# Performance work log

Measured on AMD Instinct MI355X. Metric: run time of the kernel, lower is better.

## Reference

```python
import jax, jax.numpy as jnp
import numpy as np

DIM = 1024
N_HEADS = 16
HEAD_DIM = DIM // N_HEADS
ROPE_BASE = 10000.0


def setup_inputs() -> dict:
    key = jax.random.key(0)
    ks = jax.random.split(key, 5)
    B, T = 4, 2048
    s_in = 1.0 / np.sqrt(DIM)
    x = jax.random.normal(ks[0], (B, T, DIM), dtype=jnp.float32)
    W_qkv = jax.random.uniform(ks[1], (DIM, 3 * DIM), jnp.float32, -s_in, s_in)
    b_qkv = jax.random.uniform(ks[2], (3 * DIM,), jnp.float32, -s_in, s_in)
    W_proj = jax.random.uniform(ks[3], (DIM, DIM), jnp.float32, -s_in, s_in)
    b_proj = jax.random.uniform(ks[4], (DIM,), jnp.float32, -s_in, s_in)
    return {"x": x, "W_qkv": W_qkv, "b_qkv": b_qkv, "W_proj": W_proj, "b_proj": b_proj}


def _rope_cos_sin(T, dtype):
    inv_freq = 1.0 / (ROPE_BASE ** (jnp.arange(0, HEAD_DIM, 2, dtype=jnp.float32) / HEAD_DIM))
    t = jnp.arange(T, dtype=jnp.float32)
    freqs = jnp.outer(t, inv_freq)            # (T, HEAD_DIM/2)
    emb = jnp.concatenate([freqs, freqs], -1)  # (T, HEAD_DIM)
    return jnp.cos(emb).astype(dtype), jnp.sin(emb).astype(dtype)


def _rotate_half(x):
    x1, x2 = jnp.split(x, 2, axis=-1)
    return jnp.concatenate([-x2, x1], axis=-1)


def reference(x, W_qkv, b_qkv, W_proj, b_proj):
    B, T, C = x.shape
    qkv = x @ W_qkv + b_qkv                              # (B, T, 3C)
    qkv = qkv.reshape(B, T, 3, N_HEADS, HEAD_DIM)
    qkv = jnp.transpose(qkv, (2, 0, 3, 1, 4))            # (3, B, H, T, d)
    q, k, v = qkv[0], qkv[1], qkv[2]
    cos, sin = _rope_cos_sin(T, x.dtype)
    cos = cos[None, None]                                # (1,1,T,d)
    sin = sin[None, None]
    q = q * cos + _rotate_half(q) * sin
    k = k * cos + _rotate_half(k) * sin
    scale = 1.0 / np.sqrt(HEAD_DIM)
    scores = jnp.einsum('bhqd,bhkd->bhqk', q, k) * scale  # (B,H,T,T)
    attn = jax.nn.softmax(scores, axis=-1)
    out = jnp.einsum('bhqk,bhkd->bhqd', attn, v)          # (B,H,T,d)
    out = jnp.transpose(out, (0, 2, 1, 3)).reshape(B, T, C)
    return out @ W_proj + b_proj
```

## Files before the change

### kernel.cpp

```cpp
#include <hip/hip_runtime.h>
#include <hip/hip_bf16.h>
#include <cstdint>
#include <cstddef>

typedef __bf16 bf16x8 __attribute__((ext_vector_type(8)));
typedef float f32x4 __attribute__((ext_vector_type(4)));
typedef float f32x16 __attribute__((ext_vector_type(16)));
typedef unsigned short ushort8 __attribute__((ext_vector_type(8)));

#define MFMA16(a, b, c) __builtin_amdgcn_mfma_f32_16x16x32_bf16(a, b, c, 0, 0, 0)
#define MFMA32(a, b, c) __builtin_amdgcn_mfma_f32_32x32x16_bf16(a, b, c, 0, 0, 0)

__device__ __forceinline__ void gll16(const void* g, void* l) {
  __builtin_amdgcn_global_load_lds((__attribute__((address_space(1))) unsigned int*)g,
                                   (__attribute__((address_space(3))) unsigned int*)l,
                                   16, 0, 0);
}

__device__ __forceinline__ float exp2_raw(float x) {
  return __builtin_amdgcn_exp2f(x);
}

__device__ __forceinline__ bf16x8 pack8(float a0, float a1, float a2, float a3,
                                        float a4, float a5, float a6, float a7) {
  unsigned w0, w1, w2, w3;
  asm("v_cvt_pk_bf16_f32 %0, %1, %2" : "=v"(w0) : "v"(a0), "v"(a1));
  asm("v_cvt_pk_bf16_f32 %0, %1, %2" : "=v"(w1) : "v"(a2), "v"(a3));
  asm("v_cvt_pk_bf16_f32 %0, %1, %2" : "=v"(w2) : "v"(a4), "v"(a5));
  asm("v_cvt_pk_bf16_f32 %0, %1, %2" : "=v"(w3) : "v"(a6), "v"(a7));
  asm("v_permlane32_swap_b32 %0, %1" : "+v"(w0), "+v"(w2));
  asm("v_permlane32_swap_b32 %0, %1" : "+v"(w1), "+v"(w3));
  union { unsigned u[4]; bf16x8 v; } r;
  r.u[0] = w0; r.u[1] = w1; r.u[2] = w2; r.u[3] = w3;
  return r.v;
}


__global__ void cvt_x(const float* __restrict__ in, __bf16* __restrict__ out) {
  int i = (blockIdx.x * 256 + threadIdx.x) * 8;
  float4 a = *(const float4*)(in + i);
  float4 c = *(const float4*)(in + i + 4);
  bf16x8 r;
  r[0] = (__bf16)a.x; r[1] = (__bf16)a.y; r[2] = (__bf16)a.z; r[3] = (__bf16)a.w;
  r[4] = (__bf16)c.x; r[5] = (__bf16)c.y; r[6] = (__bf16)c.z; r[7] = (__bf16)c.w;
  *(bf16x8*)(out + i) = r;
}

__global__ void rope_tab_k(float2* __restrict__ tab) {
  int i = blockIdx.x * 256 + threadIdx.x;
  int t = i >> 5, ii = i & 31;
  float invf = exp2f(-(float)ii * (13.287712379549449f / 32.0f));
  float a = (float)t * invf;
  tab[i] = make_float2(cosf(a), sinf(a));
}

__global__ void transp_bf16(const float* __restrict__ W, __bf16* __restrict__ Wt,
                            int K, int N) {
  __shared__ float tile[32][33];
  int n0 = blockIdx.x * 32, k0 = blockIdx.y * 32;
  int tx = threadIdx.x & 31, ty = threadIdx.x >> 5;
  #pragma unroll
  for (int r = ty; r < 32; r += 8)
    tile[r][tx] = W[(size_t)(k0 + r) * N + n0 + tx];
  __syncthreads();
  #pragma unroll
  for (int r = ty; r < 32; r += 8)
    Wt[(size_t)(n0 + r) * K + k0 + tx] = (__bf16)tile[tx][r];
}

__global__ void transp_v(const __bf16* __restrict__ in, __bf16* __restrict__ out) {
  __shared__ unsigned short tile[64][72];
  const int bh = blockIdx.y, t0 = blockIdx.x * 64;
  const int tid = threadIdx.x;
  const int r = tid >> 3, c = (tid & 7) * 8;
  const __bf16* src = in + ((size_t)bh * 2048 + t0) * 64;
  ushort8 a = *(const ushort8*)(src + (size_t)r * 64 + c);
  ushort8 b = *(const ushort8*)(src + (size_t)(r + 32) * 64 + c);
  #pragma unroll
  for (int e = 0; e < 8; ++e) { tile[c + e][r] = a[e]; tile[c + e][r + 32] = b[e]; }
  __syncthreads();
  const int d = tid >> 3, tc = tid & 7;
  __bf16* dst0 = out + ((size_t)bh * 64 + d) * 2048 + t0;
  *(ushort8*)(dst0 + tc * 8) = *(const ushort8*)&tile[d][tc * 8];
  __bf16* dst1 = out + ((size_t)bh * 64 + d + 32) * 2048 + t0;
  *(ushort8*)(dst1 + tc * 8) = *(const ushort8*)&tile[d + 32][tc * 8];
}

template <int EPI>
__global__ __launch_bounds__(256, 4) void gemm_bt(
    const __bf16* __restrict__ A, const __bf16* __restrict__ Bt,
    const float* __restrict__ bias, float* __restrict__ Cf,
    __bf16* __restrict__ qp, __bf16* __restrict__ kp, __bf16* __restrict__ vp,
    const float2* __restrict__ ctab, int M, int N, int K) {
  __shared__ __align__(16) char smem[32768];
  const int tid = threadIdx.x;
  const int w = tid >> 6, l = tid & 63, l15 = l & 15, g = l >> 4;
  const int wr = w >> 1, wc = w & 1;
  const int brow = blockIdx.y * 128, bcol = blockIdx.x * 128;

  f32x4 acc[4][4] = {};
  const int rsub = tid >> 3;
  const int sf   = (rsub & 7) ^ (((rsub >> 3) & 3) << 1);
  const int schunk = (((tid & 7) ^ sf) << 4);

  const int fr0 = (l15 & 7) ^ (((l15 >> 3) & 3) << 1);
  const int fr1 = (l15 & 7) ^ ((((l15 >> 3) + 2) & 3) << 1);

  for (int kt = 0; kt < K; kt += 64) {
    __syncthreads();
    #pragma unroll
    for (int i = 0; i < 4; ++i) {
      const char* ga = (const char*)(A + (size_t)(brow + i * 32 + rsub) * K + kt) + schunk;
      gll16(ga, smem + i * 4096 + tid * 16);
      const char* gb = (const char*)(Bt + (size_t)(bcol + i * 32 + rsub) * K + kt) + schunk;
      gll16(gb, smem + 16384 + i * 4096 + tid * 16);
    }
    __syncthreads();
    #pragma unroll
    for (int kk = 0; kk < 2; ++kk) {
      bf16x8 af[4], bfr[4];
      #pragma unroll
      for (int m = 0; m < 4; ++m) {
        int fx = (m & 1) ? fr1 : fr0;
        af[m] = *(const bf16x8*)(smem + (wr * 64 + m * 16 + l15) * 128 +
                                 (((kk * 4 + g) ^ fx) << 4));
      }
      #pragma unroll
      for (int n = 0; n < 4; ++n) {
        int fx = (n & 1) ? fr1 : fr0;
        bfr[n] = *(const bf16x8*)(smem + 16384 + (wc * 64 + n * 16 + l15) * 128 +
                                  (((kk * 4 + g) ^ fx) << 4));
      }
      __builtin_amdgcn_s_setprio(1);
      #pragma unroll
      for (int m = 0; m < 4; ++m)
        #pragma unroll
        for (int n = 0; n < 4; ++n)
          acc[m][n] = MFMA16(af[m], bfr[n], acc[m][n]);
      __builtin_amdgcn_s_setprio(0);
    }
  }

  const int colb = bcol + wc * 64;
  float bs[4];
  #pragma unroll
  for (int n = 0; n < 4; ++n) bs[n] = bias[colb + n * 16 + l15];

  if (EPI == 1) {
    #pragma unroll
    for (int m = 0; m < 4; ++m)
      #pragma unroll
      for (int j = 0; j < 4; ++j) {
        int row = brow + wr * 64 + m * 16 + g * 4 + j;
        float* crow = Cf + (size_t)row * N + colb;
        #pragma unroll
        for (int n = 0; n < 4; ++n)
          crow[n * 16 + l15] = acc[m][n][j] + bs[n];
      }
  } else {
    const int which = colb >> 10;
    const int h = (colb & 1023) >> 6;
    __bf16* dst = (which == 0) ? qp : (which == 1) ? kp : vp;
    const float SCLQ = 0.18033688011112042f;
    #pragma unroll
    for (int m = 0; m < 4; ++m)
      #pragma unroll
      for (int j = 0; j < 4; ++j) {
        int row = brow + wr * 64 + m * 16 + g * 4 + j;
        int bb = row >> 11, t = row & 2047;
        float v0 = acc[m][0][j] + bs[0];
        float v1 = acc[m][1][j] + bs[1];
        float v2 = acc[m][2][j] + bs[2];
        float v3 = acc[m][3][j] + bs[3];
        if (which < 2) {
          float2 cs0 = ctab[t * 32 + l15];
          float2 cs1 = ctab[t * 32 + 16 + l15];
          float r0 = v0 * cs0.x - v2 * cs0.y;
          float r2 = v2 * cs0.x + v0 * cs0.y;
          float r1 = v1 * cs1.x - v3 * cs1.y;
          float r3 = v3 * cs1.x + v1 * cs1.y;
          v0 = r0; v1 = r1; v2 = r2; v3 = r3;
        }
        if (which == 0) { v0 *= SCLQ; v1 *= SCLQ; v2 *= SCLQ; v3 *= SCLQ; }
        __bf16* orow = dst + ((size_t)(bb * 16 + h) * 2048 + t) * 64;
        orow[l15]      = (__bf16)v0;
        orow[16 + l15] = (__bf16)v1;
        orow[32 + l15] = (__bf16)v2;
        orow[48 + l15] = (__bf16)v3;
      }
  }
}

__global__ __launch_bounds__(256, 4) void flash_attn(
    const __bf16* __restrict__ q, const __bf16* __restrict__ k,
    const __bf16* __restrict__ vt, __bf16* __restrict__ o) {
  __shared__ __align__(16) char smem[32768];
  const int id = blockIdx.x;
  const int nid = (id & 7) * 128 + (id >> 3);
  const int bh = nid >> 4, qb = nid & 15;
  const int b = bh >> 4, h = bh & 15;
  const int tid = threadIdx.x, w = tid >> 6, l = tid & 63;
  const int l31 = l & 31, hi = l >> 5;

  const char* kbase  = (const char*)(k  + (size_t)bh * 2048 * 64);
  const char* vtbase = (const char*)(vt + (size_t)bh * 64 * 2048);

  bf16x8 qf[4];
  const int qrow0 = qb * 128 + w * 32;
  #pragma unroll
  for (int ks = 0; ks < 4; ++ks)
    qf[ks] = *(const bf16x8*)(q + (size_t)bh * 2048 * 64 +
                              (size_t)(qrow0 + l31) * 64 + ks * 16 + hi * 8);

  f32x16 accO[2] = {};
  float lr = 0.f;

  const int koff[2] = { 0, 16384 };
  const int voff[2] = { 8192, 24576 };

  const int srow = tid >> 3;
  const int ssw  = (((tid & 7) ^ ((tid >> 3) & 7) ^ (((tid >> 6) & 3) << 1)) << 4);
  const int swz  = (((l & 7) ^ (((l >> 3) & 3) << 1)) << 4);

  gll16(kbase + srow * 128 + ssw,                  smem + koff[0] + tid * 16);
  gll16(kbase + (srow + 32) * 128 + ssw,           smem + koff[0] + 4096 + tid * 16);
  gll16(vtbase + (size_t)srow * 4096 + ssw,        smem + voff[0] + tid * 16);
  gll16(vtbase + (size_t)(srow + 32) * 4096 + ssw, smem + voff[0] + 4096 + tid * 16);
  __syncthreads();

  for (int t = 0; t < 32; ++t) {
    const int cur = t & 1;
    char* Kc = smem + koff[cur];
    char* Vc = smem + voff[cur];
    if (t < 31) {
      char* Kn = smem + koff[cur ^ 1];
      char* Vn = smem + voff[cur ^ 1];
      const char* gk = kbase + (size_t)(t + 1) * 8192;
      gll16(gk + srow * 128 + ssw,        Kn + tid * 16);
      gll16(gk + (srow + 32) * 128 + ssw, Kn + 4096 + tid * 16);
      const char* gv = vtbase + (size_t)(t + 1) * 128;
      gll16(gv + (size_t)srow * 4096 + ssw,        Vn + tid * 16);
      gll16(gv + (size_t)(srow + 32) * 4096 + ssw, Vn + 4096 + tid * 16);
    }

    f32x16 st0 = {}, st1 = {};
    __builtin_amdgcn_s_setprio(1);
    #pragma unroll
    for (int ks = 0; ks < 4; ++ks) {
      bf16x8 kf0 = *(const bf16x8*)(Kc + (l31) * 128 + ((ks * 32 + hi * 16) ^ swz));
      bf16x8 kf1 = *(const bf16x8*)(Kc + (32 + l31) * 128 + ((ks * 32 + hi * 16) ^ swz));
      st0 = MFMA32(kf0, qf[ks], st0);
      st1 = MFMA32(kf1, qf[ks], st1);
    }
    __builtin_amdgcn_s_setprio(0);

    bf16x8 pa[4];
    {
      float p[16];
      #pragma unroll
      for (int r = 0; r < 16; ++r) p[r] = exp2_raw(st0[r]);
      lr += (((p[0] + p[1]) + (p[2] + p[3])) + ((p[4] + p[5]) + (p[6] + p[7]))) +
            (((p[8] + p[9]) + (p[10] + p[11])) + ((p[12] + p[13]) + (p[14] + p[15])));
      pa[0] = pack8(p[0], p[1], p[2], p[3], p[4], p[5], p[6], p[7]);
      pa[1] = pack8(p[8], p[9], p[10], p[11], p[12], p[13], p[14], p[15]);
    }
    {
      float p[16];
      #pragma unroll
      for (int r = 0; r < 16; ++r) p[r] = exp2_raw(st1[r]);
      lr += (((p[0] + p[1]) + (p[2] + p[3])) + ((p[4] + p[5]) + (p[6] + p[7]))) +
            (((p[8] + p[9]) + (p[10] + p[11])) + ((p[12] + p[13]) + (p[14] + p[15])));
      pa[2] = pack8(p[0], p[1], p[2], p[3], p[4], p[5], p[6], p[7]);
      pa[3] = pack8(p[8], p[9], p[10], p[11], p[12], p[13], p[14], p[15]);
    }

    __builtin_amdgcn_s_setprio(1);
    #pragma unroll
    for (int ks = 0; ks < 4; ++ks) {
      bf16x8 vf0 = *(const bf16x8*)(Vc + (l31) * 128 + ((ks * 32 + hi * 16) ^ swz));
      bf16x8 vf1 = *(const bf16x8*)(Vc + (32 + l31) * 128 + ((ks * 32 + hi * 16) ^ swz));
      accO[0] = MFMA32(pa[ks], vf0, accO[0]);
      accO[1] = MFMA32(pa[ks], vf1, accO[1]);
    }
    __builtin_amdgcn_s_setprio(0);
    __syncthreads();
  }

  float lrf = lr + __shfl_xor(lr, 32);
  __bf16* obase = o + (size_t)(b * 2048) * 1024 + h * 64;
  #pragma unroll
  for (int r = 0; r < 16; ++r) {
    int qloc = (r & 3) + 8 * (r >> 2) + 4 * hi;
    float inv = 1.0f / __shfl(lrf, qloc);
    __bf16* orow = obase + (size_t)(qrow0 + qloc) * 1024;
    orow[l31]      = (__bf16)(accO[0][r] * inv);
    orow[32 + l31] = (__bf16)(accO[1][r] * inv);
  }
}


extern "C" void kernel_launch(void* const* d_in, const int* in_sizes, int n_in,
                              void* d_out, int out_size, void* d_ws, size_t ws_size,
                              hipStream_t stream) {
  const float* x     = (const float*)d_in[0];
  const float* Wqkv  = (const float*)d_in[1];
  const float* bqkv  = (const float*)d_in[2];
  const float* Wproj = (const float*)d_in[3];
  const float* bproj = (const float*)d_in[4];
  float* out = (float*)d_out;

  char* ws = (char*)d_ws;
  __bf16* xb  = (__bf16*)(ws);
  __bf16* wtq = (__bf16*)(ws + 16777216);
  __bf16* wtp = (__bf16*)(ws + 23068672);
  __bf16* qp  = (__bf16*)(ws + 25165824);
  __bf16* kp  = (__bf16*)(ws + 41943040);
  __bf16* vp  = (__bf16*)(ws + 58720256);
  __bf16* ao  = (__bf16*)(ws + 75497472);
  float2* ct  = (float2*)(ws + 92274688);
  __bf16* vtp = xb;
  if (ws_size < 92798976) return;

  cvt_x<<<4096, 256, 0, stream>>>(x, xb);
  rope_tab_k<<<256, 256, 0, stream>>>(ct);
  transp_bf16<<<dim3(96, 32), 256, 0, stream>>>(Wqkv, wtq, 1024, 3072);
  transp_bf16<<<dim3(32, 32), 256, 0, stream>>>(Wproj, wtp, 1024, 1024);
  gemm_bt<0><<<dim3(24, 64), 256, 0, stream>>>(xb, wtq, bqkv, nullptr, qp, kp, vp, ct,
                                               8192, 3072, 1024);
  transp_v<<<dim3(32, 64), 256, 0, stream>>>(vp, vtp);
  flash_attn<<<1024, 256, 0, stream>>>(qp, kp, vtp, ao);
  gemm_bt<1><<<dim3(8, 64), 256, 0, stream>>>(ao, wtp, bproj, out, nullptr, nullptr,
                                              nullptr, nullptr, 8192, 1024, 1024);
}
```

Measured before the change: 196.0 us.

## Replace QKV GEMM with 256x256 8-wave ping-pong pipelined kernel

Adds a new QKV projection GEMM that uses 256x256 tiles, 512 threads and 128 KB of dynamic LDS split into two buffers. Each buffer holds 64-wide K tiles in quadrant halves, and loads for upcoming tiles are interleaved with MFMA compute on the current quadrants under explicit barriers and vmcnt waits. It also remaps workgroup IDs across 8 groups (XCD-aware) and raises MFMA priority. The goal is more data reuse per tile and hiding global-to-LDS latency. In exchange, occupancy drops to one block per CU and the grid shrinks to 384 blocks, which may cause tail or underfill effects on 256 CUs.

```diff
diff --git a/kernel.cpp b/kernel.cpp
--- a/kernel.cpp
+++ b/kernel.cpp
@@ -86,6 +86,184 @@
   *(ushort8*)(dst1 + tc * 8) = *(const ushort8*)&tile[d + 32][tc * 8];
 }
 
+
+template <int QM, int QN>
+__device__ __forceinline__ void compute_quad(
+    const char* buf, f32x4 (&acc)[2][2][2][4],
+    int wrp, int wcp, int l15, int g, int fr0, int fr1) {
+  const char* Ar = buf + QM * 16384;
+  const char* Br = buf + 32768 + QN * 16384;
+  bf16x8 af[2][2], bfr[4][2];
+  #pragma unroll
+  for (int m = 0; m < 2; ++m) {
+    int fx = (m & 1) ? fr1 : fr0;
+    #pragma unroll
+    for (int kk = 0; kk < 2; ++kk)
+      af[m][kk] = *(const bf16x8*)(Ar + (wrp * 32 + m * 16 + l15) * 128 +
+                                   (((kk * 4 + g) ^ fx) << 4));
+  }
+  #pragma unroll
+  for (int n = 0; n < 4; ++n) {
+    int fx = (n & 1) ? fr1 : fr0;
+    #pragma unroll
+    for (int kk = 0; kk < 2; ++kk)
+      bfr[n][kk] = *(const bf16x8*)(Br + (wcp * 64 + n * 16 + l15) * 128 +
+                                    (((kk * 4 + g) ^ fx) << 4));
+  }
+  __builtin_amdgcn_s_setprio(1);
+  #pragma unroll
+  for (int kk = 0; kk < 2; ++kk)
+    #pragma unroll
+    for (int m = 0; m < 2; ++m)
+      #pragma unroll
+      for (int n = 0; n < 4; ++n)
+        acc[QM][QN][m][n] = MFMA16(af[m][kk], bfr[n][kk], acc[QM][QN][m][n]);
+  __builtin_amdgcn_s_setprio(0);
+}
+
+template <int EPI>
+__global__ __launch_bounds__(512, 1) void gemm8p(
+    const __bf16* __restrict__ A, const __bf16* __restrict__ Bt,
+    const float* __restrict__ bias, float* __restrict__ Cf,
+    __bf16* __restrict__ qp, __bf16* __restrict__ kp, __bf16* __restrict__ vp,
+    const float2* __restrict__ ctab, int M, int N, int K) {
+  extern __shared__ __align__(16) char smem[];
+  const int tid = threadIdx.x;
+  const int w = tid >> 6, l = tid & 63, l15 = l & 15, g = l >> 4;
+  const int wrp = w & 3;
+  const int wcp = w >> 2;
+
+  const int nbx = gridDim.x;
+  const int nwg = nbx * gridDim.y;
+  const int orig = blockIdx.y * nbx + blockIdx.x;
+  const int wgid = (orig & 7) * (nwg >> 3) + (orig >> 3);
+  const int brow = (wgid / nbx) * 256, bcol = (wgid % nbx) * 256;
+
+  const int NT = K >> 6, NITER = NT >> 1;
+
+  const int srow = tid >> 3;
+  const int sf = ((tid >> 3) & 7) ^ (((tid >> 6) & 3) << 1);
+  const int schunk = ((tid & 7) ^ sf) << 4;
+  const size_t K2 = (size_t)K * 2;
+
+  const int fr0 = (l15 & 7) ^ (((l15 >> 3) & 3) << 1);
+  const int fr1 = (l15 & 7) ^ ((((l15 >> 3) + 2) & 3) << 1);
+
+  f32x4 acc[2][2][2][4] = {};
+
+#define STAGE_A8(tile, half, bufoff) do {                                              \
+    const char* _s = (const char*)A +                                                  \
+      ((size_t)(brow + (half) * 128 + srow) * K + (tile) * 64) * 2 + schunk;           \
+    gll16(_s, smem + (bufoff) + (half) * 16384 + tid * 16);                            \
+    gll16(_s + 64 * K2, smem + (bufoff) + (half) * 16384 + 8192 + tid * 16);           \
+  } while (0)
+#define STAGE_B8(tile, half, bufoff) do {                                              \
+    const char* _s = (const char*)Bt +                                                 \
+      ((size_t)(bcol + (half) * 128 + srow) * K + (tile) * 64) * 2 + schunk;           \
+    gll16(_s, smem + (bufoff) + 32768 + (half) * 16384 + tid * 16);                    \
+    gll16(_s + 64 * K2, smem + (bufoff) + 32768 + (half) * 16384 + 8192 + tid * 16);   \
+  } while (0)
+#define BARRIER() do { asm volatile("" ::: "memory");                                  \
+    __builtin_amdgcn_s_barrier(); asm volatile("" ::: "memory"); } while (0)
+
+  STAGE_A8(0, 0, 0); STAGE_B8(0, 0, 0); STAGE_A8(0, 1, 0); STAGE_B8(0, 1, 0);
+  STAGE_A8(1, 0, 65536); STAGE_B8(1, 0, 65536);
+
+  for (int it = 0; it < NITER; ++it) {
+    const int t = it * 2;
+    const bool more2 = (t + 2 < NT), more3 = (t + 3 < NT);
+    asm volatile("s_waitcnt vmcnt(4)" ::: "memory");
+    BARRIER();
+    STAGE_A8(t + 1, 1, 65536);
+    compute_quad<0, 0>(smem, acc, wrp, wcp, l15, g, fr0, fr1);
+    BARRIER();
+    STAGE_B8(t + 1, 1, 65536);
+    compute_quad<0, 1>(smem, acc, wrp, wcp, l15, g, fr0, fr1);
+    BARRIER();
+    if (more2) STAGE_A8(t + 2, 0, 0);
+    compute_quad<1, 0>(smem, acc, wrp, wcp, l15, g, fr0, fr1);
+    BARRIER();
+    if (more2) STAGE_B8(t + 2, 0, 0);
+    compute_quad<1, 1>(smem, acc, wrp, wcp, l15, g, fr0, fr1);
+    BARRIER();
+    if (it == NITER - 1) { asm volatile("s_waitcnt vmcnt(0)" ::: "memory"); }
+    else                 { asm volatile("s_waitcnt vmcnt(4)" ::: "memory"); }
+    BARRIER();
+    if (more2) STAGE_A8(t + 2, 1, 0);
+    compute_quad<0, 0>(smem + 65536, acc, wrp, wcp, l15, g, fr0, fr1);
+    BARRIER();
+    if (more2) STAGE_B8(t + 2, 1, 0);
+    compute_quad<0, 1>(smem + 65536, acc, wrp, wcp, l15, g, fr0, fr1);
+    BARRIER();
+    if (more3) STAGE_A8(t + 3, 0, 65536);
+    compute_quad<1, 0>(smem + 65536, acc, wrp, wcp, l15, g, fr0, fr1);
+    BARRIER();
+    if (more3) STAGE_B8(t + 3, 0, 65536);
+    compute_quad<1, 1>(smem + 65536, acc, wrp, wcp, l15, g, fr0, fr1);
+    BARRIER();
+  }
+#undef STAGE_A8
+#undef STAGE_B8
+#undef BARRIER
+
+  #pragma unroll
+  for (int qn = 0; qn < 2; ++qn) {
+    const int colb = bcol + qn * 128 + wcp * 64;
+    float bs[4];
+    #pragma unroll
+    for (int n = 0; n < 4; ++n) bs[n] = bias[colb + n * 16 + l15];
+    if (EPI == 1) {
+      #pragma unroll
+      for (int qm = 0; qm < 2; ++qm)
+        #pragma unroll
+        for (int m = 0; m < 2; ++m)
+          #pragma unroll
+          for (int j = 0; j < 4; ++j) {
+            int row = brow + qm * 128 + wrp * 32 + m * 16 + g * 4 + j;
+            float* crow = Cf + (size_t)row * N + colb;
+            #pragma unroll
+            for (int n = 0; n < 4; ++n)
+              crow[n * 16 + l15] = acc[qm][qn][m][n][j] + bs[n];
+          }
+    } else {
+      const int which = colb >> 10;
+      const int h = (colb & 1023) >> 6;
+      __bf16* dst = (which == 0) ? qp : (which == 1) ? kp : vp;
+      const float SCLQ = 0.18033688011112042f;
+      #pragma unroll
+      for (int qm = 0; qm < 2; ++qm)
+        #pragma unroll
+        for (int m = 0; m < 2; ++m)
+          #pragma unroll
+          for (int j = 0; j < 4; ++j) {
+            int row = brow + qm * 128 + wrp * 32 + m * 16 + g * 4 + j;
+            int bb = row >> 11, t = row & 2047;
+            float v0 = acc[qm][qn][0][m * 0 + 0][j];
+            (void)v0;
+            float a0 = acc[qm][qn][m][0][j] + bs[0];
+            float a1 = acc[qm][qn][m][1][j] + bs[1];
+            float a2 = acc[qm][qn][m][2][j] + bs[2];
+            float a3 = acc[qm][qn][m][3][j] + bs[3];
+            if (which < 2) {
+              float2 cs0 = ctab[t * 32 + l15];
+              float2 cs1 = ctab[t * 32 + 16 + l15];
+              float r0 = a0 * cs0.x - a2 * cs0.y;
+              float r2 = a2 * cs0.x + a0 * cs0.y;
+              float r1 = a1 * cs1.x - a3 * cs1.y;
+              float r3 = a3 * cs1.x + a1 * cs1.y;
+              a0 = r0; a1 = r1; a2 = r2; a3 = r3;
+            }
+            if (which == 0) { a0 *= SCLQ; a1 *= SCLQ; a2 *= SCLQ; a3 *= SCLQ; }
+            __bf16* orow = dst + ((size_t)(bb * 16 + h) * 2048 + t) * 64;
+            orow[l15]      = (__bf16)a0;
+            orow[16 + l15] = (__bf16)a1;
+            orow[32 + l15] = (__bf16)a2;
+            orow[48 + l15] = (__bf16)a3;
+          }
+    }
+  }
+}
+
 template <int EPI>
 __global__ __launch_bounds__(256, 4) void gemm_bt(
     const __bf16* __restrict__ A, const __bf16* __restrict__ Bt,
@@ -102,7 +280,6 @@
   const int rsub = tid >> 3;
   const int sf   = (rsub & 7) ^ (((rsub >> 3) & 3) << 1);
   const int schunk = (((tid & 7) ^ sf) << 4);
-
   const int fr0 = (l15 & 7) ^ (((l15 >> 3) & 3) << 1);
   const int fr1 = (l15 & 7) ^ ((((l15 >> 3) + 2) & 3) << 1);
 
@@ -321,12 +498,16 @@
   __bf16* vtp = xb;
   if (ws_size < 92798976) return;
 
+  const int LDS8P = 131072;
+  hipFuncSetAttribute((const void*)gemm8p<0>,
+                      hipFuncAttributeMaxDynamicSharedMemorySize, LDS8P);
+
   cvt_x<<<4096, 256, 0, stream>>>(x, xb);
   rope_tab_k<<<256, 256, 0, stream>>>(ct);
   transp_bf16<<<dim3(96, 32), 256, 0, stream>>>(Wqkv, wtq, 1024, 3072);
   transp_bf16<<<dim3(32, 32), 256, 0, stream>>>(Wproj, wtp, 1024, 1024);
-  gemm_bt<0><<<dim3(24, 64), 256, 0, stream>>>(xb, wtq, bqkv, nullptr, qp, kp, vp, ct,
-                                               8192, 3072, 1024);
+  gemm8p<0><<<dim3(12, 32), 512, LDS8P, stream>>>(xb, wtq, bqkv, nullptr,
+                                                  qp, kp, vp, ct, 8192, 3072, 1024);
   transp_v<<<dim3(32, 64), 256, 0, stream>>>(vp, vtp);
   flash_attn<<<1024, 256, 0, stream>>>(qp, kp, vtp, ao);
   gemm_bt<1><<<dim3(8, 64), 256, 0, stream>>>(ao, wtp, bproj, out, nullptr, nullptr,
```

Result: slower. 212.3 us (median of 2 runs) (+8.3%).

## Fuse V transpose into QKV GEMM epilogue and merge prep kernels

Applied to the files above, without the earlier changes.

The V part of the QKV GEMM epilogue now stages the tile in shared memory with an XOR swizzle and writes V already transposed, so the separate transp_v kernel is gone. The RoPE table build is folded into the x conversion kernel, and the two weight transposes are merged into one launch. This removes three kernel launches and one full read and write of V, at the cost of an extra shared-memory round trip and two barriers in the V epilogue blocks.

```diff
diff --git a/kernel.cpp b/kernel.cpp
--- a/kernel.cpp
+++ b/kernel.cpp
@@ -36,7 +36,8 @@
 }
 
 
-__global__ void cvt_x(const float* __restrict__ in, __bf16* __restrict__ out) {
+__global__ void cvt_x(const float* __restrict__ in, __bf16* __restrict__ out,
+                      float2* __restrict__ tab) {
   int i = (blockIdx.x * 256 + threadIdx.x) * 8;
   float4 a = *(const float4*)(in + i);
   float4 c = *(const float4*)(in + i + 4);
@@ -44,20 +45,24 @@
   r[0] = (__bf16)a.x; r[1] = (__bf16)a.y; r[2] = (__bf16)a.z; r[3] = (__bf16)a.w;
   r[4] = (__bf16)c.x; r[5] = (__bf16)c.y; r[6] = (__bf16)c.z; r[7] = (__bf16)c.w;
   *(bf16x8*)(out + i) = r;
-}
-
-__global__ void rope_tab_k(float2* __restrict__ tab) {
-  int i = blockIdx.x * 256 + threadIdx.x;
-  int t = i >> 5, ii = i & 31;
-  float invf = exp2f(-(float)ii * (13.287712379549449f / 32.0f));
-  float a = (float)t * invf;
-  tab[i] = make_float2(cosf(a), sinf(a));
-}
-
-__global__ void transp_bf16(const float* __restrict__ W, __bf16* __restrict__ Wt,
-                            int K, int N) {
+  if (blockIdx.x < 256) {
+    int idx = blockIdx.x * 256 + threadIdx.x;
+    int t = idx >> 5, ii = idx & 31;
+    float invf = exp2f(-(float)ii * (13.287712379549449f / 32.0f));
+    float ang = (float)t * invf;
+    tab[idx] = make_float2(cosf(ang), sinf(ang));
+  }
+}
+
+__global__ void transp_w(const float* __restrict__ Wq, __bf16* __restrict__ Wtq,
+                         const float* __restrict__ Wp, __bf16* __restrict__ Wtp) {
   __shared__ float tile[32][33];
-  int n0 = blockIdx.x * 32, k0 = blockIdx.y * 32;
+  int bx = blockIdx.x;
+  const float* W; __bf16* Wt; int N;
+  if (bx < 96) { W = Wq; Wt = Wtq; N = 3072; }
+  else         { W = Wp; Wt = Wtp; N = 1024; bx -= 96; }
+  const int K = 1024;
+  int n0 = bx * 32, k0 = blockIdx.y * 32;
   int tx = threadIdx.x & 31, ty = threadIdx.x >> 5;
   #pragma unroll
   for (int r = ty; r < 32; r += 8)
@@ -66,31 +71,13 @@
   #pragma unroll
   for (int r = ty; r < 32; r += 8)
     Wt[(size_t)(n0 + r) * K + k0 + tx] = (__bf16)tile[tx][r];
-}
-
-__global__ void transp_v(const __bf16* __restrict__ in, __bf16* __restrict__ out) {
-  __shared__ unsigned short tile[64][72];
-  const int bh = blockIdx.y, t0 = blockIdx.x * 64;
-  const int tid = threadIdx.x;
-  const int r = tid >> 3, c = (tid & 7) * 8;
-  const __bf16* src = in + ((size_t)bh * 2048 + t0) * 64;
-  ushort8 a = *(const ushort8*)(src + (size_t)r * 64 + c);
-  ushort8 b = *(const ushort8*)(src + (size_t)(r + 32) * 64 + c);
-  #pragma unroll
-  for (int e = 0; e < 8; ++e) { tile[c + e][r] = a[e]; tile[c + e][r + 32] = b[e]; }
-  __syncthreads();
-  const int d = tid >> 3, tc = tid & 7;
-  __bf16* dst0 = out + ((size_t)bh * 64 + d) * 2048 + t0;
-  *(ushort8*)(dst0 + tc * 8) = *(const ushort8*)&tile[d][tc * 8];
-  __bf16* dst1 = out + ((size_t)bh * 64 + d + 32) * 2048 + t0;
-  *(ushort8*)(dst1 + tc * 8) = *(const ushort8*)&tile[d + 32][tc * 8];
 }
 
 template <int EPI>
 __global__ __launch_bounds__(256, 4) void gemm_bt(
     const __bf16* __restrict__ A, const __bf16* __restrict__ Bt,
     const float* __restrict__ bias, float* __restrict__ Cf,
-    __bf16* __restrict__ qp, __bf16* __restrict__ kp, __bf16* __restrict__ vp,
+    __bf16* __restrict__ qp, __bf16* __restrict__ kp, __bf16* __restrict__ vtp,
     const float2* __restrict__ ctab, int M, int N, int K) {
   __shared__ __align__(16) char smem[32768];
   const int tid = threadIdx.x;
@@ -102,7 +89,6 @@
   const int rsub = tid >> 3;
   const int sf   = (rsub & 7) ^ (((rsub >> 3) & 3) << 1);
   const int schunk = (((tid & 7) ^ sf) << 4);
-
   const int fr0 = (l15 & 7) ^ (((l15 >> 3) & 3) << 1);
   const int fr1 = (l15 & 7) ^ ((((l15 >> 3) + 2) & 3) << 1);
 
@@ -159,20 +145,20 @@
       }
   } else {
     const int which = colb >> 10;
-    const int h = (colb & 1023) >> 6;
-    __bf16* dst = (which == 0) ? qp : (which == 1) ? kp : vp;
-    const float SCLQ = 0.18033688011112042f;
-    #pragma unroll
-    for (int m = 0; m < 4; ++m)
-      #pragma unroll
-      for (int j = 0; j < 4; ++j) {
-        int row = brow + wr * 64 + m * 16 + g * 4 + j;
-        int bb = row >> 11, t = row & 2047;
-        float v0 = acc[m][0][j] + bs[0];
-        float v1 = acc[m][1][j] + bs[1];
-        float v2 = acc[m][2][j] + bs[2];
-        float v3 = acc[m][3][j] + bs[3];
-        if (which < 2) {
+    if (which < 2) {
+      const int h = (colb & 1023) >> 6;
+      __bf16* dst = (which == 0) ? qp : kp;
+      const float SCLQ = 0.18033688011112042f;
+      #pragma unroll
+      for (int m = 0; m < 4; ++m)
+        #pragma unroll
+        for (int j = 0; j < 4; ++j) {
+          int row = brow + wr * 64 + m * 16 + g * 4 + j;
+          int bb = row >> 11, t = row & 2047;
+          float v0 = acc[m][0][j] + bs[0];
+          float v1 = acc[m][1][j] + bs[1];
+          float v2 = acc[m][2][j] + bs[2];
+          float v3 = acc[m][3][j] + bs[3];
           float2 cs0 = ctab[t * 32 + l15];
           float2 cs1 = ctab[t * 32 + 16 + l15];
           float r0 = v0 * cs0.x - v2 * cs0.y;
@@ -180,14 +166,41 @@
           float r1 = v1 * cs1.x - v3 * cs1.y;
           float r3 = v3 * cs1.x + v1 * cs1.y;
           v0 = r0; v1 = r1; v2 = r2; v3 = r3;
+          if (which == 0) { v0 *= SCLQ; v1 *= SCLQ; v2 *= SCLQ; v3 *= SCLQ; }
+          __bf16* orow = dst + ((size_t)(bb * 16 + h) * 2048 + t) * 64;
+          orow[l15]      = (__bf16)v0;
+          orow[16 + l15] = (__bf16)v1;
+          orow[32 + l15] = (__bf16)v2;
+          orow[48 + l15] = (__bf16)v3;
         }
-        if (which == 0) { v0 *= SCLQ; v1 *= SCLQ; v2 *= SCLQ; v3 *= SCLQ; }
-        __bf16* orow = dst + ((size_t)(bb * 16 + h) * 2048 + t) * 64;
-        orow[l15]      = (__bf16)v0;
-        orow[16 + l15] = (__bf16)v1;
-        orow[32 + l15] = (__bf16)v2;
-        orow[48 + l15] = (__bf16)v3;
-      }
+    } else {
+      __syncthreads();
+      #pragma unroll
+      for (int n = 0; n < 4; ++n) {
+        int cloc = wc * 64 + n * 16 + l15;
+        char* cbase = smem + cloc * 256;
+        int sw = (cloc & 15) << 4;
+        #pragma unroll
+        for (int m = 0; m < 4; ++m)
+          #pragma unroll
+          for (int j = 0; j < 4; ++j) {
+            int rloc = wr * 64 + m * 16 + g * 4 + j;
+            *(__bf16*)(cbase + ((rloc * 2) ^ sw)) = (__bf16)(acc[m][n][j] + bs[n]);
+          }
+      }
+      __syncthreads();
+      const int b = brow >> 11, t0 = brow & 2047;
+      const int h0 = (bcol - 2048) >> 6;
+      const int tch = l & 15;
+      #pragma unroll
+      for (int i = 0; i < 8; ++i) {
+        int c = w * 32 + i * 4 + (l >> 4);
+        ushort8 vrow = *(const ushort8*)(smem + c * 256 + ((tch * 16) ^ ((c & 15) << 4)));
+        __bf16* dst = vtp + ((size_t)((b * 16 + h0 + (c >> 6)) * 64 + (c & 63)) * 2048 +
+                             t0 + tch * 8);
+        *(ushort8*)dst = vrow;
+      }
+    }
   }
 }
 
@@ -315,19 +328,15 @@
   __bf16* wtp = (__bf16*)(ws + 23068672);
   __bf16* qp  = (__bf16*)(ws + 25165824);
   __bf16* kp  = (__bf16*)(ws + 41943040);
-  __bf16* vp  = (__bf16*)(ws + 58720256);
+  __bf16* vtp = (__bf16*)(ws + 58720256);
   __bf16* ao  = (__bf16*)(ws + 75497472);
   float2* ct  = (float2*)(ws + 92274688);
-  __bf16* vtp = xb;
   if (ws_size < 92798976) return;
 
-  cvt_x<<<4096, 256, 0, stream>>>(x, xb);
-  rope_tab_k<<<256, 256, 0, stream>>>(ct);
-  transp_bf16<<<dim3(96, 32), 256, 0, stream>>>(Wqkv, wtq, 1024, 3072);
-  transp_bf16<<<dim3(32, 32), 256, 0, stream>>>(Wproj, wtp, 1024, 1024);
-  gemm_bt<0><<<dim3(24, 64), 256, 0, stream>>>(xb, wtq, bqkv, nullptr, qp, kp, vp, ct,
+  cvt_x<<<4096, 256, 0, stream>>>(x, xb, ct);
+  transp_w<<<dim3(128, 32), 256, 0, stream>>>(Wqkv, wtq, Wproj, wtp);
+  gemm_bt<0><<<dim3(24, 64), 256, 0, stream>>>(xb, wtq, bqkv, nullptr, qp, kp, vtp, ct,
                                                8192, 3072, 1024);
-  transp_v<<<dim3(32, 64), 256, 0, stream>>>(vp, vtp);
   flash_attn<<<1024, 256, 0, stream>>>(qp, kp, vtp, ao);
   gemm_bt<1><<<dim3(8, 64), 256, 0, stream>>>(ao, wtp, bproj, out, nullptr, nullptr,
                                               nullptr, nullptr, 8192, 1024, 1024);
```

Result: faster. 177.1 us, median of 2 (-9.6%).
